# Optimization experiments

Hardware: AMD Instinct MI355X
Metric: run time of the kernel (lower is better)

## Reference

```python
import jax, jax.numpy as jnp
import numpy as np
from functools import partial

N = 100000
E = 1600000
F_IN, F_HID, F_OUT = 128, 128, 64


def setup_inputs() -> dict:
    key = jax.random.key(0)
    ks = jax.random.split(key, 10)
    x = jax.random.normal(ks[0], (N, F_IN), dtype=jnp.float32)
    edge_index = jax.random.randint(ks[1], (2, E), 0, N, dtype=jnp.int64)
    edge_attr = jax.random.uniform(ks[2], (E,), dtype=jnp.float32)
    # GCNConv params: Linear(in, out, bias=False) weight + separate bias
    def glorot(k, fan_in, fan_out):
        lim = jnp.sqrt(6.0 / (fan_in + fan_out))
        return jax.random.uniform(k, (fan_in, fan_out), minval=-lim, maxval=lim, dtype=jnp.float32)
    return {
        "x": x, "edge_index": edge_index, "edge_attr": edge_attr,
        "W1": glorot(ks[3], F_IN, F_HID),  "b1": jnp.zeros((F_HID,), jnp.float32),
        "W2": glorot(ks[4], F_HID, F_HID), "b2": jnp.zeros((F_HID,), jnp.float32),
        "W3": glorot(ks[5], F_HID, F_OUT), "b3": jnp.zeros((F_OUT,), jnp.float32),
    }


def _gcn_norm(src, dst, ew, n):
    # PyG gcn_norm: add self-loops with weight 1, symmetric normalization.
    loop = jnp.arange(n, dtype=src.dtype)
    src_f = jnp.concatenate([src, loop])
    dst_f = jnp.concatenate([dst, loop])
    ew_f = jnp.concatenate([ew, jnp.ones((n,), ew.dtype)])
    deg = jax.ops.segment_sum(ew_f, dst_f, num_segments=n)
    dinv = jnp.where(deg > 0, jax.lax.rsqrt(deg), 0.0)
    norm = dinv[src_f] * ew_f * dinv[dst_f]  # [E+N]
    return src_f, dst_f, norm


def _gcn_conv(x, W, b, src_f, dst_f, norm, n):
    h = x @ W  # [N, out]
    msg = norm[:, None] * h[src_f]  # gather + per-edge scale
    out = jax.ops.segment_sum(msg, dst_f, num_segments=n)  # scatter-add
    return out + b


def reference(x, edge_index, edge_attr, W1, b1, W2, b2, W3, b3):
    n = x.shape[0]
    src, dst = edge_index[0], edge_index[1]
    src_f, dst_f, norm = _gcn_norm(src, dst, edge_attr, n)
    h = jax.nn.relu(_gcn_conv(x, W1, b1, src_f, dst_f, norm, n))
    h = jax.nn.relu(_gcn_conv(h, W2, b2, src_f, dst_f, norm, n))
    out = _gcn_conv(h, W3, b3, src_f, dst_f, norm, n)
    return jax.nn.log_softmax(out, axis=-1)
```

## Files before the change

### kernel.cpp

```cpp
#include <hip/hip_runtime.h>

typedef unsigned short ushortT;
typedef unsigned int uintT;
typedef unsigned long long ullT;
typedef __attribute__((ext_vector_type(8))) short bf16x8;
typedef __attribute__((ext_vector_type(4))) float f32x4;

#define NBUCK 391
#define EPB   4096
#define NBEB  391
#define BSLOT 4608

union H16 { ushortT u; _Float16 h; };

__device__ __forceinline__ float bf2f(uintT u16) {
    return __uint_as_float(u16 << 16);
}
__device__ __forceinline__ float bflo(uintT u) {
    return __uint_as_float(u << 16);
}
__device__ __forceinline__ float bfhi(uintT u) {
    return __uint_as_float(u & 0xffff0000u);
}
__device__ __forceinline__ ushortT f2bf(float f) {
    unsigned int u = __float_as_uint(f);
    unsigned int r = (u + 0x7fffu + ((u >> 16) & 1u)) >> 16;
    return (ushortT)r;
}

#define ACC8(U, W) \
    acc[0] = fmaf(W, bflo(U.x), acc[0]); acc[1] = fmaf(W, bfhi(U.x), acc[1]); \
    acc[2] = fmaf(W, bflo(U.y), acc[2]); acc[3] = fmaf(W, bfhi(U.y), acc[3]); \
    acc[4] = fmaf(W, bflo(U.z), acc[4]); acc[5] = fmaf(W, bfhi(U.z), acc[5]); \
    acc[6] = fmaf(W, bflo(U.w), acc[6]); acc[7] = fmaf(W, bfhi(U.w), acc[7]);


__device__ __forceinline__ void twist_body(const float* W, ushortT* Wt, int K, int C, int idx) {
    if (idx < K * C) {
        int k = idx / C, c = idx - k * C;
        Wt[c * K + k] = f2bf(W[idx]);
    }
}

template <int C, bool ABF16>
__device__ __forceinline__ void gemm_body(const void* Aop, const ushortT* Wt,
                                          ushortT* outp, int nrows, int bid, int tid) {
    const int K = 128;
    int wv = tid >> 6;
    int ln = tid & 63;
    int row0 = (bid * 4 + wv) * 16;
    if (row0 >= nrows) return;
    int rA = ln & 15;
    int kg = ln >> 4;
    int rowA = row0 + rA;
    bool okA = rowA < nrows;

    bf16x8 af[4];
    if (ABF16) {
        const ushortT* A = (const ushortT*)Aop;
        #pragma unroll
        for (int kb = 0; kb < 4; ++kb) {
            if (okA) af[kb] = *(const bf16x8*)(A + (size_t)rowA * K + kb * 32 + kg * 8);
            else     af[kb] = (bf16x8)(short)0;
        }
    } else {
        const float* A = (const float*)Aop;
        #pragma unroll
        for (int kb = 0; kb < 4; ++kb) {
            bf16x8 t = (bf16x8)(short)0;
            if (okA) {
                const float4* ap = reinterpret_cast<const float4*>(A + (size_t)rowA * K + kb * 32 + kg * 8);
                float4 p0 = ap[0], p1 = ap[1];
                t[0] = (short)f2bf(p0.x); t[1] = (short)f2bf(p0.y);
                t[2] = (short)f2bf(p0.z); t[3] = (short)f2bf(p0.w);
                t[4] = (short)f2bf(p1.x); t[5] = (short)f2bf(p1.y);
                t[6] = (short)f2bf(p1.z); t[7] = (short)f2bf(p1.w);
            }
            af[kb] = t;
        }
    }

    int colB = ln & 15;
    f32x4 acc[C / 16];
    #pragma unroll
    for (int nt = 0; nt < C / 16; ++nt) acc[nt] = (f32x4)0.0f;
    #pragma unroll
    for (int nt = 0; nt < C / 16; ++nt) {
        int c = nt * 16 + colB;
        #pragma unroll
        for (int kb = 0; kb < 4; ++kb) {
            bf16x8 bfr = *(const bf16x8*)(Wt + c * K + kb * 32 + kg * 8);
            acc[nt] = __builtin_amdgcn_mfma_f32_16x16x32_bf16(af[kb], bfr, acc[nt], 0, 0, 0);
        }
    }
    #pragma unroll
    for (int nt = 0; nt < C / 16; ++nt) {
        #pragma unroll
        for (int r = 0; r < 4; ++r) {
            int rowC = row0 + (ln >> 4) * 4 + r;
            if (rowC < nrows) outp[(size_t)rowC * C + nt * 16 + colB] = f2bf(acc[nt][r]);
        }
    }
}

__global__ __launch_bounds__(512) void k_sort_twist(const int* src, const int* dst, const float* ew,
                                                    int* bucket_count, ullT* erec, int e,
                                                    const float* W1, ushortT* Wt1,
                                                    const float* W2, ushortT* Wt2,
                                                    const float* W3, ushortT* Wt3) {
    __shared__ ullT srec[EPB];
    __shared__ int  gaddr[EPB];
    __shared__ int  hist[512];
    __shared__ int  adj[NBUCK];
    int blk = blockIdx.x, t = threadIdx.x;
    if (blk >= NBEB) {
        int tb = blk - NBEB;
        if (tb < 32)      twist_body(W1, Wt1, 128, 128, tb * 512 + t);
        else if (tb < 64) twist_body(W2, Wt2, 128, 128, (tb - 32) * 512 + t);
        else              twist_body(W3, Wt3, 128, 64, (tb - 64) * 512 + t);
        return;
    }
    hist[t] = 0;
    __syncthreads();
    int base = blk * EPB;
    for (int j = t; j < EPB; j += 512) {
        int i = base + j;
        if (i < e) atomicAdd(&hist[dst[i] >> 8], 1);
    }
    __syncthreads();
    int myc = hist[t];
    for (int off = 1; off < 512; off <<= 1) {
        int x = 0; if (t >= off) x = hist[t - off];
        __syncthreads();
        if (t >= off) hist[t] += x;
        __syncthreads();
    }
    int lb = (t == 0) ? 0 : hist[t - 1];
    __syncthreads();
    hist[t] = lb;
    if (t < NBUCK) {
        int gb = 0;
        if (myc > 0) gb = atomicAdd(&bucket_count[t], myc);
        adj[t] = t * BSLOT + gb - lb;
    }
    __syncthreads();
    for (int j = t; j < EPB; j += 512) {
        int i = base + j;
        if (i < e) {
            int d = dst[i];
            int b = d >> 8;
            int pos = atomicAdd(&hist[b], 1);
            H16 cv; cv.h = (_Float16)ew[i];
            ullT rec = ((ullT)(uintT)src[i] << 24) | ((ullT)(uintT)(d & 255) << 16) | (ullT)cv.u;
            srec[pos] = rec;
            int ga = adj[b] + pos;
            int lim = b * BSLOT + BSLOT - 1;
            gaddr[pos] = ga <= lim ? ga : lim;
        }
    }
    __syncthreads();
    int m = e - base; if (m > EPB) m = EPB;
    for (int k = t; k < m; k += 512) {
        erec[(size_t)gaddr[k]] = srec[k];
    }
}

__global__ __launch_bounds__(256) void k_bucket_gemm1(const ullT* erec,
                                                      const int* bucket_count,
                                                      uintT* entries, float* dinv, int* counts, int n,
                                                      const float* x, const ushortT* Wt1,
                                                      ushortT* hw1) {
    __shared__ int cnt[256];
    __shared__ uintT wsum[256];
    int blk = blockIdx.x, t = threadIdx.x;
    if (blk < NBUCK) {
        int b = blk;
        cnt[t] = 0; wsum[t] = 0;
        __syncthreads();
        int beg = b * BSLOT, m = bucket_count[b];
        if (m > BSLOT) m = BSLOT;
        for (int j = t; j < m; j += 256) {
            ullT rec = erec[(size_t)beg + j];
            int dlow = (int)((rec >> 16) & 255);
            ushortT hu = (ushortT)(rec & 0xffffu);
            int slot = atomicAdd(&cnt[dlow], 1);
            H16 cv; cv.u = hu;
            atomicAdd(&wsum[dlow], (uintT)__float2uint_rn((float)cv.h * 16777216.0f));
            if (slot < 64) {
                uintT s = (uintT)(rec >> 24);
                entries[((size_t)b * 256 + dlow) * 64 + slot] = (s << 15) | (uintT)hu;
            }
        }
        __syncthreads();
        int node = b * 256 + t;
        if (node < n) {
            float sum = (float)wsum[t] * (1.0f / 16777216.0f);
            dinv[node] = rsqrtf(1.0f + sum);
            int c = cnt[t];
            counts[node] = c > 64 ? 64 : c;
        }
    } else {
        gemm_body<128, false>(x, Wt1, hw1, n, blk - NBUCK, t);
    }
}

template <int C>
__global__ __launch_bounds__(256) void k_agg_gemm(const char* hwb, const float* dinv,
                                                  const int* counts, const uintT* entries,
                                                  const float* bias, const ushortT* Wt,
                                                  ushortT* outp, int n) {
    __shared__ ullT wp[4][64];
    __shared__ uintT rows[4][16][64];
    int wv = threadIdx.x >> 6, ln = threadIdx.x & 63;
    int tile0 = (blockIdx.x * 4 + wv) * 16;
    if (tile0 >= n) return;
    int lg = ln & 15;
    int gp = ln >> 4;

    const char* lane_base = hwb + (size_t)(lg * 16);
    float2 bs = *(const float2*)(bias + 2 * (lg * 4 + gp));

    float wfac_n = dinv[tile0];
    int   cnt_n  = counts[tile0];
    uintT ent_n  = entries[(size_t)tile0 * 64 + ln];
    float wsrc_n = dinv[(int)(ent_n >> 15)];

    #pragma unroll 1
    for (int nn = 0; nn < 16; ++nn) {
        int i = tile0 + nn;
        float wfac = wfac_n;
        int cnt = cnt_n;
        uintT ent = ent_n;
        float wsrc = wsrc_n;
        if (nn < 15) {
            wfac_n = dinv[i + 1];
            cnt_n  = counts[i + 1];
            ent_n  = entries[(size_t)(i + 1) * 64 + ln];
            wsrc_n = dinv[(int)(ent_n >> 15)];
        }
        int cntp = (cnt + 7) & ~7;
        H16 cv; cv.u = (ushortT)(ent & 0x7fffu);
        float w_l = (ln < cnt) ? wsrc * (float)cv.h * wfac : 0.f;
        uintT soff = (ln < cnt) ? ((ent >> 15) << 8) : 0u;
        wp[wv][ln] = ((ullT)__float_as_uint(w_l) << 32) | (ullT)soff;
        const ullT* wpw = wp[wv];

        uint4 uself = *(const uint4*)(lane_base + (size_t)i * 256);

        float acc[8];
        #pragma unroll
        for (int j = 0; j < 8; ++j) acc[j] = 0.f;

        ullT pa = wpw[gp], pb = wpw[4 + gp];
        uint4 ua = *(const uint4*)(lane_base + (uintT)pa);
        uint4 ub = *(const uint4*)(lane_base + (uintT)pb);
        for (int e = 8; e < cntp; e += 8) {
            ullT pa2 = wpw[e + gp], pb2 = wpw[e + 4 + gp];
            uint4 ua2 = *(const uint4*)(lane_base + (uintT)pa2);
            uint4 ub2 = *(const uint4*)(lane_base + (uintT)pb2);
            float wa = __uint_as_float((uintT)(pa >> 32));
            float wb = __uint_as_float((uintT)(pb >> 32));
            ACC8(ua, wa)
            ACC8(ub, wb)
            pa = pa2; pb = pb2; ua = ua2; ub = ub2;
        }
        {
            float wa = __uint_as_float((uintT)(pa >> 32));
            float wb = __uint_as_float((uintT)(pb >> 32));
            ACC8(ua, wa)
            ACC8(ub, wb)
        }

        #pragma unroll
        for (int j = 0; j < 8; ++j) {
            acc[j] += __shfl_xor(acc[j], 16);
            acc[j] += __shfl_xor(acc[j], 32);
        }
        float selfw = wfac * wfac;
        ACC8(uself, selfw)

        float a0 = (gp & 1) ? ((gp & 2) ? acc[6] : acc[2]) : ((gp & 2) ? acc[4] : acc[0]);
        float a1 = (gp & 1) ? ((gp & 2) ? acc[7] : acc[3]) : ((gp & 2) ? acc[5] : acc[1]);
        a0 = fmaxf(a0 + bs.x, 0.f);
        a1 = fmaxf(a1 + bs.y, 0.f);
        uintT packed = (uintT)f2bf(a0) | ((uintT)f2bf(a1) << 16);
        rows[wv][nn][(((lg * 4 + gp) * 4) ^ ((nn & 7) << 4)) >> 2] = packed;
    }
    asm volatile("s_waitcnt lgkmcnt(0)" ::: "memory");

    {
        int rA = ln & 15;
        int kg = ln >> 4;
        int colB = ln & 15;
        const char* rbase = (const char*)&rows[wv][0][0];
        bf16x8 af[4];
        #pragma unroll
        for (int kb = 0; kb < 4; ++kb) {
            int byteoff = (kb * 64 + kg * 16) ^ ((rA & 7) << 4);
            af[kb] = *(const bf16x8*)(rbase + rA * 256 + byteoff);
        }
        #pragma unroll
        for (int nt = 0; nt < C / 16; ++nt) {
            f32x4 gac = (f32x4)0.0f;
            int c = nt * 16 + colB;
            #pragma unroll
            for (int kb = 0; kb < 4; ++kb) {
                bf16x8 bfr = *(const bf16x8*)(Wt + c * 128 + kb * 32 + kg * 8);
                gac = __builtin_amdgcn_mfma_f32_16x16x32_bf16(af[kb], bfr, gac, 0, 0, 0);
            }
            #pragma unroll
            for (int r = 0; r < 4; ++r) {
                int rowC = tile0 + kg * 4 + r;
                outp[(size_t)rowC * C + nt * 16 + colB] = f2bf(gac[r]);
            }
        }
    }
}

__global__ __launch_bounds__(256) void k_agg_softmax(const char* hwb, const float* dinv,
                                                     const int* counts, const uintT* entries,
                                                     const float* bias, float* outp, int n) {
    __shared__ ullT wp[4][64];
    int wv = threadIdx.x >> 6, ln = threadIdx.x & 63;
    int i = blockIdx.x * 4 + wv;
    if (i >= n) return;
    int lg = ln & 7;
    int gp = ln >> 3;

    float wfac = dinv[i];
    int cnt = counts[i];
    int cntp = (cnt + 7) & ~7;
    uintT ent = entries[(size_t)i * 64 + ln];
    int s_l = (ln < cnt) ? (int)(ent >> 15) : 0;
    H16 cv; cv.u = (ushortT)(ent & 0x7fffu);
    float w_l = (ln < cnt) ? dinv[s_l] * (float)cv.h * wfac : 0.f;
    wp[wv][ln] = ((ullT)__float_as_uint(w_l) << 32) | (ullT)((uintT)s_l << 7);
    const ullT* wpw = wp[wv];

    const char* lane_base = hwb + (size_t)(lg * 16);
    uint4 uself = *(const uint4*)(lane_base + (size_t)i * 128);

    float acc[8];
    #pragma unroll
    for (int j = 0; j < 8; ++j) acc[j] = 0.f;

    ullT pa = wpw[gp];
    uint4 ua = *(const uint4*)(lane_base + (uintT)pa);
    for (int e = 8; e < cntp; e += 8) {
        ullT pa2 = wpw[e + gp];
        uint4 ua2 = *(const uint4*)(lane_base + (uintT)pa2);
        float wa = __uint_as_float((uintT)(pa >> 32));
        ACC8(ua, wa)
        pa = pa2; ua = ua2;
    }
    {
        float wa = __uint_as_float((uintT)(pa >> 32));
        ACC8(ua, wa)
    }

    #pragma unroll
    for (int j = 0; j < 8; ++j) {
        acc[j] += __shfl_xor(acc[j], 8);
        acc[j] += __shfl_xor(acc[j], 16);
        acc[j] += __shfl_xor(acc[j], 32);
    }
    float selfw = wfac * wfac;
    ACC8(uself, selfw)

    float4 bsa = *(const float4*)(bias + lg * 8);
    float4 bsb = *(const float4*)(bias + lg * 8 + 4);
    acc[0] += bsa.x; acc[1] += bsa.y; acc[2] += bsa.z; acc[3] += bsa.w;
    acc[4] += bsb.x; acc[5] += bsb.y; acc[6] += bsb.z; acc[7] += bsb.w;

    float m = acc[0];
    #pragma unroll
    for (int j = 1; j < 8; ++j) m = fmaxf(m, acc[j]);
    m = fmaxf(m, __shfl_xor(m, 1));
    m = fmaxf(m, __shfl_xor(m, 2));
    m = fmaxf(m, __shfl_xor(m, 4));
    float s = 0.f;
    #pragma unroll
    for (int j = 0; j < 8; ++j) s += __expf(acc[j] - m);
    s += __shfl_xor(s, 1);
    s += __shfl_xor(s, 2);
    s += __shfl_xor(s, 4);
    float ls = m + __logf(s);

    float v0 = (gp & 1) ? acc[4] : acc[0];
    float v1 = (gp & 1) ? acc[5] : acc[1];
    float v2 = (gp & 1) ? acc[6] : acc[2];
    float v3 = (gp & 1) ? acc[7] : acc[3];
    if (gp < 2) {
        float4 r = { v0 - ls, v1 - ls, v2 - ls, v3 - ls };
        *(float4*)(outp + (size_t)i * 64 + lg * 8 + gp * 4) = r;
    }
}

extern "C" void kernel_launch(void* const* d_in, const int* in_sizes, int n_in,
                              void* d_out, int out_size, void* d_ws, size_t ws_size,
                              hipStream_t stream) {
    const int N = 100000, E = 1600000;
    const int NPAD = NBUCK * 256;
    const float* x  = (const float*)d_in[0];
    const int*   src = (const int*)d_in[1];
    const int*   dst = src + E;
    const float* ea = (const float*)d_in[2];
    const float* W1 = (const float*)d_in[3];
    const float* b1 = (const float*)d_in[4];
    const float* W2 = (const float*)d_in[5];
    const float* b2 = (const float*)d_in[6];
    const float* W3 = (const float*)d_in[7];
    const float* b3 = (const float*)d_in[8];
    float* outp = (float*)d_out;

    char* ws = (char*)d_ws;
    auto alloc = [&](size_t bytes) {
        char* p = ws;
        ws += (bytes + 255) & ~(size_t)255;
        return p;
    };
    int*   bucket_count = (int*)alloc((size_t)NBUCK * 4);
    ullT*  erec         = (ullT*)alloc((size_t)NBUCK * BSLOT * 8);
    float* dinv    = (float*)alloc((size_t)N * 4);
    int*   counts  = (int*)  alloc((size_t)N * 4);
    uintT* entries = (uintT*)alloc((size_t)NPAD * 64 * 4);
    ushortT* Wt1   = (ushortT*)alloc(128 * 128 * 2);
    ushortT* Wt2   = (ushortT*)alloc(128 * 128 * 2);
    ushortT* Wt3   = (ushortT*)alloc(128 * 64 * 2);
    ushortT* hwA   = (ushortT*)alloc((size_t)N * 128 * 2);
    ushortT* hwB   = (ushortT*)alloc((size_t)N * 128 * 2);

    const int nbGemm = (N + 63) / 64;
    const int nbTile = N / 16;
    const int nbFused = (nbTile + 3) / 4;
    const int nbAgg  = (N + 3) / 4;

    hipMemsetAsync(bucket_count, 0, (size_t)NBUCK * 4, stream);
    k_sort_twist<<<NBEB + 80, 512, 0, stream>>>(src, dst, ea, bucket_count, erec, E,
                                                W1, Wt1, W2, Wt2, W3, Wt3);
    k_bucket_gemm1<<<NBUCK + nbGemm, 256, 0, stream>>>(erec, bucket_count,
                                                       entries, dinv, counts, N,
                                                       x, Wt1, hwA);
    k_agg_gemm<128><<<nbFused, 256, 0, stream>>>((const char*)hwA, dinv, counts, entries,
                                                 b1, Wt2, hwB, N);
    k_agg_gemm<64><<<nbFused, 256, 0, stream>>>((const char*)hwB, dinv, counts, entries,
                                                b2, Wt3, hwA, N);
    k_agg_softmax<<<nbAgg, 256, 0, stream>>>((const char*)hwA, dinv, counts, entries,
                                             b3, outp, N);
}
```

Before: 384.0 us.

## Share 16-node tile across block waves with dynamic row claiming and split GEMM columns

Each block now processes a single 16-node tile instead of four. The four waves claim rows dynamically through an LDS atomic counter, which balances uneven neighbor counts. After a block barrier, the waves split the MFMA output columns of the shared tile between them. This is meant to cut per-wave load imbalance and raise block count, at the cost of LDS atomics, a __syncthreads, and four times more blocks.

```diff
diff --git a/kernel.cpp b/kernel.cpp
--- a/kernel.cpp
+++ b/kernel.cpp
@@ -210,34 +210,49 @@
                                                   const float* bias, const ushortT* Wt,
                                                   ushortT* outp, int n) {
     __shared__ ullT wp[4][64];
-    __shared__ uintT rows[4][16][64];
+    __shared__ uintT rows[16][64];
+    __shared__ int cur;
     int wv = threadIdx.x >> 6, ln = threadIdx.x & 63;
-    int tile0 = (blockIdx.x * 4 + wv) * 16;
-    if (tile0 >= n) return;
+    int tile0 = blockIdx.x * 16;
     int lg = ln & 15;
     int gp = ln >> 4;
 
+    if (threadIdx.x == 0) cur = 0;
+    __syncthreads();
+
     const char* lane_base = hwb + (size_t)(lg * 16);
     float2 bs = *(const float2*)(bias + 2 * (lg * 4 + gp));
 
-    float wfac_n = dinv[tile0];
-    int   cnt_n  = counts[tile0];
-    uintT ent_n  = entries[(size_t)tile0 * 64 + ln];
-    float wsrc_n = dinv[(int)(ent_n >> 15)];
-
-    #pragma unroll 1
-    for (int nn = 0; nn < 16; ++nn) {
-        int i = tile0 + nn;
+    int r_n = 0;
+    if (ln == 0) r_n = atomicAdd(&cur, 1);
+    r_n = __shfl(r_n, 0);
+    float wfac_n = 0.f, wsrc_n = 0.f;
+    int cnt_n = 0; uintT ent_n = 0;
+    if (r_n < 16) {
+        int i = tile0 + r_n;
+        wfac_n = dinv[i];
+        cnt_n  = counts[i];
+        ent_n  = entries[(size_t)i * 64 + ln];
+        wsrc_n = dinv[(int)(ent_n >> 15)];
+    }
+
+    while (r_n < 16) {
+        int r = r_n;
+        int i = tile0 + r;
         float wfac = wfac_n;
         int cnt = cnt_n;
         uintT ent = ent_n;
         float wsrc = wsrc_n;
-        if (nn < 15) {
-            wfac_n = dinv[i + 1];
-            cnt_n  = counts[i + 1];
-            ent_n  = entries[(size_t)(i + 1) * 64 + ln];
+        if (ln == 0) r_n = atomicAdd(&cur, 1);
+        r_n = __shfl(r_n, 0);
+        if (r_n < 16) {
+            int i2 = tile0 + r_n;
+            wfac_n = dinv[i2];
+            cnt_n  = counts[i2];
+            ent_n  = entries[(size_t)i2 * 64 + ln];
             wsrc_n = dinv[(int)(ent_n >> 15)];
         }
+
         int cntp = (cnt + 7) & ~7;
         H16 cv; cv.u = (ushortT)(ent & 0x7fffu);
         float w_l = (ln < cnt) ? wsrc * (float)cv.h * wfac : 0.f;
@@ -284,23 +299,25 @@
         a0 = fmaxf(a0 + bs.x, 0.f);
         a1 = fmaxf(a1 + bs.y, 0.f);
         uintT packed = (uintT)f2bf(a0) | ((uintT)f2bf(a1) << 16);
-        rows[wv][nn][(((lg * 4 + gp) * 4) ^ ((nn & 7) << 4)) >> 2] = packed;
-    }
-    asm volatile("s_waitcnt lgkmcnt(0)" ::: "memory");
+        rows[r][(((lg * 4 + gp) * 4) ^ ((r & 7) << 4)) >> 2] = packed;
+    }
+    __syncthreads();
 
     {
         int rA = ln & 15;
         int kg = ln >> 4;
         int colB = ln & 15;
-        const char* rbase = (const char*)&rows[wv][0][0];
+        const char* rbase = (const char*)&rows[0][0];
         bf16x8 af[4];
         #pragma unroll
         for (int kb = 0; kb < 4; ++kb) {
             int byteoff = (kb * 64 + kg * 16) ^ ((rA & 7) << 4);
             af[kb] = *(const bf16x8*)(rbase + rA * 256 + byteoff);
         }
-        #pragma unroll
-        for (int nt = 0; nt < C / 16; ++nt) {
+        const int NS = C / 64;
+        #pragma unroll
+        for (int s = 0; s < NS; ++s) {
+            int nt = wv * NS + s;
             f32x4 gac = (f32x4)0.0f;
             int c = nt * 16 + colB;
             #pragma unroll
@@ -431,8 +448,7 @@
     ushortT* hwB   = (ushortT*)alloc((size_t)N * 128 * 2);
 
     const int nbGemm = (N + 63) / 64;
-    const int nbTile = N / 16;
-    const int nbFused = (nbTile + 3) / 4;
+    const int nbFused = N / 16;
     const int nbAgg  = (N + 3) / 4;
 
     hipMemsetAsync(bucket_count, 0, (size_t)NBUCK * 4, stream);
```

After: 362.7 us. 5.5% less time.
